# Kernel optimization log

Hardware: AMD Instinct MI355X
Metric: run time of the kernel (lower is better)

Reference implementation:

```python
import jax, jax.numpy as jnp
import numpy as np

K, N = 4096, 4096
GROUP_SIZE = 128
N_GROUPS = N // GROUP_SIZE  # 32
BATCH, SEQ = 4, 2048
NBITS = 4


def setup_inputs() -> dict:
    key = jax.random.key(0)
    ks = jax.random.split(key, 7)
    x = jax.random.normal(ks[0], (BATCH, SEQ, N), dtype=jnp.float32)
    W_q = jax.random.randint(ks[1], (K, N), 0, 2 ** NBITS, dtype=jnp.int32)
    scales = jax.random.uniform(ks[2], (K, N_GROUPS, 1), dtype=jnp.float32) * 0.05 + 0.001
    zeros = jax.random.uniform(ks[3], (K, N_GROUPS, 1), dtype=jnp.float32) * (2 ** NBITS)
    mu1 = jax.random.uniform(ks[4], (N,), dtype=jnp.float32) + 0.5  # per-column sinkhorn factor
    mu2 = jax.random.uniform(ks[5], (K,), dtype=jnp.float32) + 0.5  # per-row sinkhorn factor
    bias = jax.random.normal(ks[6], (K,), dtype=jnp.float32)
    return {"x": x, "W_q": W_q, "scales": scales, "zeros": zeros,
            "mu1": mu1, "mu2": mu2, "bias": bias}


def reference(x, W_q, scales, zeros, mu1, mu2, bias):
    input_dtype = x.dtype
    n_groups = scales.shape[1]
    group_size = W_q.shape[1] // n_groups
    # group-wise dequant: [K, n_groups, group_size]
    Q_g = W_q.astype(jnp.float32).reshape(K, n_groups, group_size)
    W_deq_norm = (Q_g - zeros) * scales
    # undo sinkhorn row/col normalization
    W_deq = W_deq_norm.reshape(K, N) * mu2[:, None] * mu1[None, :]
    W_deq = W_deq.astype(input_dtype)
    # linear: x [B,S,N] @ W_deq.T [N,K] + bias [K]
    return jnp.einsum('bsn,kn->bsk', x, W_deq) + bias
```

## Files before the change

### kernel.cpp

```cpp
#include <hip/hip_runtime.h>
#include <hip/hip_bf16.h>
#include <stdint.h>

#define M_DIM 8192
#define N_C   4096
#define K_OUT 4096
#define NGRP  32
#define NT    (N_C / 32)

typedef __attribute__((ext_vector_type(8))) short bf16x8;
typedef __attribute__((ext_vector_type(4))) float f32x4;

__device__ __forceinline__ unsigned short f2b(float f) {
  unsigned u = __float_as_uint(f);
  return (unsigned short)((u + 0x7fffu + ((u >> 16) & 1u)) >> 16);
}

__device__ __forceinline__ void gload_lds16(const void* g, void* l) {
  __builtin_amdgcn_global_load_lds(
      (const __attribute__((address_space(1))) void*)g,
      (__attribute__((address_space(3))) void*)l,
      16, 0, 0);
}

__global__ void convert_x_kernel(const float* __restrict__ x,
                                 unsigned short* __restrict__ xb) {
  const int total = (M_DIM * N_C) / 8;
  const int stride = gridDim.x * blockDim.x;
  for (int i = blockIdx.x * blockDim.x + threadIdx.x; i < total; i += stride) {
    const float4* p = (const float4*)(x + (size_t)i * 8);
    float4 a = p[0];
    float4 b = p[1];
    union { unsigned short u[8]; uint4 v; } o;
    o.u[0] = f2b(a.x); o.u[1] = f2b(a.y); o.u[2] = f2b(a.z); o.u[3] = f2b(a.w);
    o.u[4] = f2b(b.x); o.u[5] = f2b(b.y); o.u[6] = f2b(b.z); o.u[7] = f2b(b.w);
    *(uint4*)(xb + (size_t)i * 8) = o.v;
  }
}

__global__ void dequant_w_kernel(const int* __restrict__ Wq,
                                 const float* __restrict__ scales,
                                 const float* __restrict__ zeros,
                                 const float* __restrict__ mu1,
                                 const float* __restrict__ mu2,
                                 unsigned short* __restrict__ wb) {
  const int total = (K_OUT * N_C) / 8;
  const int stride = gridDim.x * blockDim.x;
  for (int i = blockIdx.x * blockDim.x + threadIdx.x; i < total; i += stride) {
    const int k  = i >> 9;
    const int nc = (i & 511) << 3;
    const int g  = nc >> 7;
    const float s = scales[k * NGRP + g];
    const float z = zeros[k * NGRP + g];
    const float f  = s * mu2[k];
    const float zf = z * f;
    const int4* q4 = (const int4*)(Wq + (size_t)k * N_C + nc);
    int4 q0 = q4[0], q1 = q4[1];
    const float4* m4 = (const float4*)(mu1 + nc);
    float4 m0 = m4[0], m1 = m4[1];
    union { unsigned short u[8]; uint4 v; } o;
    o.u[0] = f2b(((float)q0.x * f - zf) * m0.x);
    o.u[1] = f2b(((float)q0.y * f - zf) * m0.y);
    o.u[2] = f2b(((float)q0.z * f - zf) * m0.z);
    o.u[3] = f2b(((float)q0.w * f - zf) * m0.w);
    o.u[4] = f2b(((float)q1.x * f - zf) * m1.x);
    o.u[5] = f2b(((float)q1.y * f - zf) * m1.y);
    o.u[6] = f2b(((float)q1.z * f - zf) * m1.z);
    o.u[7] = f2b(((float)q1.w * f - zf) * m1.w);
    *(uint4*)(wb + (size_t)i * 8) = o.v;
  }
}

__global__ __launch_bounds__(512) void gemm_bf16_kernel(
    const unsigned short* __restrict__ Xb,
    const unsigned short* __restrict__ Wb,
    const float* __restrict__ bias,
    float* __restrict__ out) {
  __shared__ unsigned short smem[65536];

  const int bid = blockIdx.x;
  const int swz = (bid & 7) * 64 + (bid >> 3);
  const int n0 = (swz & 15) * 256;
  const int m0 = (swz >> 4) * 256;

  const int tid = threadIdx.x;
  const int w   = tid >> 6;
  const int l   = tid & 63;
  const int wr  = w >> 2;
  const int wc  = w & 3;

  const char* Xc = (const char*)Xb;
  const char* Wc = (const char*)Wb;
  const char* srcA[2];
  const char* srcB[2];
  int dstOff[2];
#pragma unroll
  for (int e = 0; e < 2; ++e) {
    const int P  = (e * 8 + w) * 1024 + l * 16;
    const int r  = P >> 6;
    const int sl = ((P >> 4) & 3) ^ ((r >> 1) & 3);
    srcA[e] = Xc + (size_t)(m0 + r) * (N_C * 2) + sl * 16;
    srcB[e] = Wc + (size_t)(n0 + r) * (N_C * 2) + sl * 16;
    dstOff[e] = (e * 8 + w) * 1024;
  }

  int offa[8], offb[4];
#pragma unroll
  for (int i = 0; i < 8; ++i) {
    const int r  = wr * 128 + i * 16 + (l & 15);
    const int sl = (l >> 4) ^ ((r >> 1) & 3);
    offa[i] = (r * 64 + sl * 16) >> 1;
  }
#pragma unroll
  for (int j = 0; j < 4; ++j) {
    const int r  = wc * 64 + j * 16 + (l & 15);
    const int sl = (l >> 4) ^ ((r >> 1) & 3);
    offb[j] = (16384 + r * 64 + sl * 16) >> 1;
  }

  f32x4 acc[8][4] = {};
  char* ldsc = (char*)smem;

#define STAGE(tt)                                                            \
  { const int sb = ((tt) & 3) * 32768; const size_t ko = (size_t)(tt) * 64;  \
    gload_lds16(srcA[0] + ko, ldsc + sb + dstOff[0]);                        \
    gload_lds16(srcA[1] + ko, ldsc + sb + dstOff[1]);                        \
    gload_lds16(srcB[0] + ko, ldsc + sb + 16384 + dstOff[0]);                \
    gload_lds16(srcB[1] + ko, ldsc + sb + 16384 + dstOff[1]); }

  STAGE(0)
  STAGE(1)
  STAGE(2)

#define KSTEP(VMSTR, tt, DOSTAGE)                                            \
  { asm volatile("s_waitcnt vmcnt(" VMSTR ")\n\ts_barrier" ::: "memory");    \
    const int bufo = ((tt) & 3) * 16384;                                     \
    bf16x8 af[8]; bf16x8 bfv[4];                                             \
    _Pragma("unroll") for (int i = 0; i < 8; ++i)                            \
      af[i] = *(const bf16x8*)(smem + bufo + offa[i]);                       \
    _Pragma("unroll") for (int j = 0; j < 4; ++j)                            \
      bfv[j] = *(const bf16x8*)(smem + bufo + offb[j]);                      \
    if (DOSTAGE) STAGE((tt) + 3)                                             \
    __builtin_amdgcn_s_setprio(1);                                           \
    _Pragma("unroll") for (int i = 0; i < 8; ++i)                            \
      _Pragma("unroll") for (int j = 0; j < 4; ++j)                          \
        acc[i][j] = __builtin_amdgcn_mfma_f32_16x16x32_bf16(af[i], bfv[j],   \
                                                            acc[i][j], 0, 0, 0); \
    __builtin_amdgcn_s_setprio(0); }

#pragma unroll 1
  for (int kt = 0; kt < NT - 3; ++kt) KSTEP("8", kt, 1)
  KSTEP("8", NT - 3, 0)
  KSTEP("4", NT - 2, 0)
  KSTEP("0", NT - 1, 0)

#undef KSTEP
#undef STAGE

#pragma unroll
  for (int j = 0; j < 4; ++j) {
    const int col = n0 + wc * 64 + j * 16 + (l & 15);
    const float bv = bias[col];
#pragma unroll
    for (int i = 0; i < 8; ++i) {
      const int row = m0 + wr * 128 + i * 16 + (l >> 4) * 4;
#pragma unroll
      for (int rr = 0; rr < 4; ++rr)
        out[(size_t)(row + rr) * K_OUT + col] = acc[i][j][rr] + bv;
    }
  }
}

extern "C" void kernel_launch(void* const* d_in, const int* in_sizes, int n_in,
                              void* d_out, int out_size, void* d_ws, size_t ws_size,
                              hipStream_t stream) {
  const float* x      = (const float*)d_in[0];
  const int*   Wq     = (const int*)d_in[1];
  const float* scales = (const float*)d_in[2];
  const float* zeros  = (const float*)d_in[3];
  const float* mu1    = (const float*)d_in[4];
  const float* mu2    = (const float*)d_in[5];
  const float* bias   = (const float*)d_in[6];
  float* out = (float*)d_out;

  unsigned short* xb = (unsigned short*)d_ws;
  unsigned short* wb = xb + (size_t)M_DIM * N_C;

  convert_x_kernel<<<2048, 256, 0, stream>>>(x, xb);
  dequant_w_kernel<<<2048, 256, 0, stream>>>(Wq, scales, zeros, mu1, mu2, wb);

  dim3 grid((M_DIM / 256) * (K_OUT / 256));
  gemm_bf16_kernel<<<grid, 512, 0, stream>>>(xb, wb, bias, out);
}
```

Before: 298.1 us.

## Shrink GEMM tile to 128x256 with triple-buffered LDS for higher occupancy

Halves the M extent of each GEMM block tile (256x256 to 128x256), doubling the grid, and cuts the LDS ring from four to three stages so the shared footprint falls from 128 KB to 72 KB. Accumulators drop from 8x4 to 4x4 MFMA tiles per wave, and launch bounds request multiple blocks per CU. The aim is more resident waves and a better-balanced grid to hide latency. The cost is lower arithmetic intensity per block (more global/L2 traffic for W) and a shallower prefetch pipeline.

```diff
diff --git a/kernel.cpp b/kernel.cpp
--- a/kernel.cpp
+++ b/kernel.cpp
@@ -71,17 +71,17 @@
   }
 }
 
-__global__ __launch_bounds__(512) void gemm_bf16_kernel(
+__global__ __launch_bounds__(512, 4) void gemm_bf16_kernel(
     const unsigned short* __restrict__ Xb,
     const unsigned short* __restrict__ Wb,
     const float* __restrict__ bias,
     float* __restrict__ out) {
-  __shared__ unsigned short smem[65536];
+  __shared__ unsigned short smem[36864];
 
   const int bid = blockIdx.x;
-  const int swz = (bid & 7) * 64 + (bid >> 3);
+  const int swz = (bid & 7) * 128 + (bid >> 3);
+  const int m0 = (swz >> 4) * 128;
   const int n0 = (swz & 15) * 256;
-  const int m0 = (swz >> 4) * 256;
 
   const int tid = threadIdx.x;
   const int w   = tid >> 6;
@@ -91,70 +91,55 @@
 
   const char* Xc = (const char*)Xb;
   const char* Wc = (const char*)Wb;
-  const char* srcA[2];
-  const char* srcB[2];
-  int dstOff[2];
-#pragma unroll
-  for (int e = 0; e < 2; ++e) {
-    const int P  = (e * 8 + w) * 1024 + l * 16;
-    const int r  = P >> 6;
-    const int sl = ((P >> 4) & 3) ^ ((r >> 1) & 3);
-    srcA[e] = Xc + (size_t)(m0 + r) * (N_C * 2) + sl * 16;
-    srcB[e] = Wc + (size_t)(n0 + r) * (N_C * 2) + sl * 16;
-    dstOff[e] = (e * 8 + w) * 1024;
-  }
-
-  int offa[8], offb[4];
-#pragma unroll
-  for (int i = 0; i < 8; ++i) {
-    const int r  = wr * 128 + i * 16 + (l & 15);
-    const int sl = (l >> 4) ^ ((r >> 1) & 3);
-    offa[i] = (r * 64 + sl * 16) >> 1;
-  }
-#pragma unroll
-  for (int j = 0; j < 4; ++j) {
-    const int r  = wc * 64 + j * 16 + (l & 15);
-    const int sl = (l >> 4) ^ ((r >> 1) & 3);
-    offb[j] = (16384 + r * 64 + sl * 16) >> 1;
-  }
-
-  f32x4 acc[8][4] = {};
   char* ldsc = (char*)smem;
 
-#define STAGE(tt)                                                            \
-  { const int sb = ((tt) & 3) * 32768; const size_t ko = (size_t)(tt) * 64;  \
-    gload_lds16(srcA[0] + ko, ldsc + sb + dstOff[0]);                        \
-    gload_lds16(srcA[1] + ko, ldsc + sb + dstOff[1]);                        \
-    gload_lds16(srcB[0] + ko, ldsc + sb + 16384 + dstOff[0]);                \
-    gload_lds16(srcB[1] + ko, ldsc + sb + 16384 + dstOff[1]); }
+  const int rS = tid >> 2;
+  const int sS = (tid & 3) ^ ((rS >> 1) & 3);
+  const unsigned voffA  = (unsigned)(m0 + rS) * 8192u + (unsigned)sS * 16u;
+  const unsigned voffB0 = (unsigned)(n0 + rS) * 8192u + (unsigned)sS * 16u;
+  const unsigned voffB1 = (unsigned)(n0 + 128 + rS) * 8192u + (unsigned)sS * 16u;
+  const int dstAu  = w * 1024;
+  const int dstB0u = 8192 + w * 1024;
+  const int dstB1u = 16384 + w * 1024;
 
-  STAGE(0)
-  STAGE(1)
-  STAGE(2)
+  const int rdA = wr * 64 + (l & 15);
+  const int offA0 = rdA * 64 + (((l >> 4) ^ ((rdA >> 1) & 3)) * 16);
+  const int rdB = wc * 64 + (l & 15);
+  const int offB0 = 8192 + rdB * 64 + (((l >> 4) ^ ((rdB >> 1) & 3)) * 16);
 
-#define KSTEP(VMSTR, tt, DOSTAGE)                                            \
+  f32x4 acc[4][4] = {};
+
+#define STAGE(tt) { char* nb = ldsc + ((tt) % 3) * 24576;                    \
+    const unsigned ko = (unsigned)(tt) * 64u;                                \
+    gload_lds16(Xc + voffA + ko,  nb + dstAu);                               \
+    gload_lds16(Wc + voffB0 + ko, nb + dstB0u);                              \
+    gload_lds16(Wc + voffB1 + ko, nb + dstB1u); }
+
+#define BODY(VMSTR, tt, DOSTAGE)                                             \
   { asm volatile("s_waitcnt vmcnt(" VMSTR ")\n\ts_barrier" ::: "memory");    \
-    const int bufo = ((tt) & 3) * 16384;                                     \
-    bf16x8 af[8]; bf16x8 bfv[4];                                             \
-    _Pragma("unroll") for (int i = 0; i < 8; ++i)                            \
-      af[i] = *(const bf16x8*)(smem + bufo + offa[i]);                       \
+    const char* bp = ldsc + ((tt) % 3) * 24576;                              \
+    bf16x8 af[4], bfv[4];                                                    \
+    _Pragma("unroll") for (int i = 0; i < 4; ++i)                            \
+      af[i] = *(const bf16x8*)(bp + offA0 + i * 1024);                       \
     _Pragma("unroll") for (int j = 0; j < 4; ++j)                            \
-      bfv[j] = *(const bf16x8*)(smem + bufo + offb[j]);                      \
-    if (DOSTAGE) STAGE((tt) + 3)                                             \
+      bfv[j] = *(const bf16x8*)(bp + offB0 + j * 1024);                      \
+    if (DOSTAGE) STAGE((tt) + 2)                                             \
     __builtin_amdgcn_s_setprio(1);                                           \
-    _Pragma("unroll") for (int i = 0; i < 8; ++i)                            \
+    _Pragma("unroll") for (int i = 0; i < 4; ++i)                            \
       _Pragma("unroll") for (int j = 0; j < 4; ++j)                          \
         acc[i][j] = __builtin_amdgcn_mfma_f32_16x16x32_bf16(af[i], bfv[j],   \
                                                             acc[i][j], 0, 0, 0); \
     __builtin_amdgcn_s_setprio(0); }
 
+  STAGE(0)
+  STAGE(1)
+
 #pragma unroll 1
-  for (int kt = 0; kt < NT - 3; ++kt) KSTEP("8", kt, 1)
-  KSTEP("8", NT - 3, 0)
-  KSTEP("4", NT - 2, 0)
-  KSTEP("0", NT - 1, 0)
+  for (int t = 0; t < NT - 2; ++t) BODY("3", t, 1)
+  BODY("3", NT - 2, 0)
+  BODY("0", NT - 1, 0)
 
-#undef KSTEP
+#undef BODY
 #undef STAGE
 
 #pragma unroll
@@ -162,8 +147,8 @@
     const int col = n0 + wc * 64 + j * 16 + (l & 15);
     const float bv = bias[col];
 #pragma unroll
-    for (int i = 0; i < 8; ++i) {
-      const int row = m0 + wr * 128 + i * 16 + (l >> 4) * 4;
+    for (int i = 0; i < 4; ++i) {
+      const int row = m0 + wr * 64 + i * 16 + (l >> 4) * 4;
 #pragma unroll
       for (int rr = 0; rr < 4; ++rr)
         out[(size_t)(row + rr) * K_OUT + col] = acc[i][j][rr] + bv;
@@ -189,6 +174,6 @@
   convert_x_kernel<<<2048, 256, 0, stream>>>(x, xb);
   dequant_w_kernel<<<2048, 256, 0, stream>>>(Wq, scales, zeros, mu1, mu2, wb);
 
-  dim3 grid((M_DIM / 256) * (K_OUT / 256));
+  dim3 grid((M_DIM / 128) * (K_OUT / 256));
   gemm_bf16_kernel<<<grid, 512, 0, stream>>>(xb, wb, bias, out);
 }
```

Result: slower. 336.0 us (+12.7%).
